# Performance work log

Measured on AMD Instinct MI355X. Metric: run time of the kernel, lower is better.

## Reference

```python
import jax, jax.numpy as jnp
import numpy as np
import math

B, T, E, H, QL, SUB = 4, 2048, 64, 8, 6, 64  # batch, win_len, n_embd, n_head, q_len, sub_len


def _row_mask(index, sub_len, win_len):
    log_l = math.ceil(np.log2(sub_len))
    mask = np.zeros(win_len, dtype=np.float32)
    if (win_len // sub_len) * 2 * log_l > index:
        mask[: index + 1] = 1
    else:
        while index >= 0:
            if index - log_l + 1 < 0:
                mask[:index] = 1
                break
            mask[index - log_l + 1 : index + 1] = 1
            for i in range(log_l):
                new_index = index - log_l + 1 - 2 ** i
                if index - new_index <= sub_len and new_index >= 0:
                    mask[new_index] = 1
            index -= sub_len
    return mask


def _log_mask(win_len, sub_len):
    m = np.zeros((win_len, win_len), dtype=np.float32)
    for i in range(win_len):
        m[i] = _row_mask(i, sub_len, win_len)
    return m.reshape(1, 1, win_len, win_len)


def setup_inputs() -> dict:
    key = jax.random.key(0)
    ks = jax.random.split(key, 4)
    x = jax.random.normal(ks[0], (B, T, E), dtype=jnp.float32)
    Wqk = jax.random.normal(ks[1], (2 * H * E, E, QL), dtype=jnp.float32) * 0.02
    bqk = jnp.zeros((2 * H * E,), dtype=jnp.float32)
    Wv = jax.random.normal(ks[2], (E, H * E), dtype=jnp.float32) * 0.02
    bv = jnp.zeros((H * E,), dtype=jnp.float32)
    Wp = jax.random.normal(ks[3], (H * E, E), dtype=jnp.float32) * 0.02
    bp = jnp.zeros((E,), dtype=jnp.float32)
    mask = jnp.asarray(_log_mask(T, SUB).astype(bool))  # [1,1,T,T] bool
    return {"x": x, "Wqk": Wqk, "bqk": bqk, "Wv": Wv, "bv": bv,
            "Wp": Wp, "bp": bp, "mask": mask}


def reference(x, Wqk, bqk, Wv, bv, Wp, bp, mask):
    b, t, e = x.shape
    h = Wv.shape[1] // e
    ql = Wqk.shape[-1]

    # value projection (Conv1D rf=1 == dense)
    value = x @ Wv + bv                              # [B,T,H*E]

    # causal conv1d QK projection: left-pad by q_len-1
    xc = jnp.transpose(x, (0, 2, 1))                 # [B,E,T]
    qk = jax.lax.conv_general_dilated(
        xc, Wqk, window_strides=(1,), padding=[(ql - 1, 0)],
        dimension_numbers=("NCH", "OIH", "NCH"))    # [B,2*H*E,T]
    qk = qk + bqk[None, :, None]
    qk = jnp.transpose(qk, (0, 2, 1))                # [B,T,2*H*E]
    query, key_ = jnp.split(qk, 2, axis=2)

    q = query.reshape(b, t, h, e).transpose(0, 2, 1, 3)   # [B,H,T,E]
    k = key_.reshape(b, t, h, e).transpose(0, 2, 3, 1)    # [B,H,E,T]
    v = value.reshape(b, t, h, e).transpose(0, 2, 1, 3)   # [B,H,T,E]

    pre = jnp.einsum("bhqe,bhek->bhqk", q, k) / jnp.sqrt(jnp.asarray(e, x.dtype))
    m = mask[:, :, :t, :t].astype(pre.dtype)
    pre = pre * m + (-1e9) * (1.0 - m)
    attn_weights = jax.nn.softmax(pre, axis=-1)           # [B,H,T,T]
    # dropout p=0.0 -> identity
    attn = jnp.einsum("bhqk,bhke->bhqe", attn_weights, v)  # [B,H,T,E]
    attn = attn.transpose(0, 2, 1, 3).reshape(b, t, h * e)
    out = attn @ Wp + bp                                  # [B,T,E]
    return out, attn_weights
```

## Files before the change

kernel.cpp:

```cpp
#include <hip/hip_runtime.h>
#include <hip/hip_bf16.h>


typedef __attribute__((ext_vector_type(8))) short bf16x8;
typedef __attribute__((ext_vector_type(4))) float f32x4;
typedef unsigned int uint32;

#define MFMA16(a, b, c) __builtin_amdgcn_mfma_f32_16x16x32_bf16((a), (b), (c), 0, 0, 0)

static __device__ __forceinline__ bool sparse_pred(int r, int c) {
  int d = r - c;
  if (d < 0) return false;
  int o = d & 63;
  int j = c + o;
  bool inS = (o <= 7) || (o == 9) || (o == 13) || (o == 21) || (o == 37);
  return (j >= 5) ? inS : (o >= 1);
}

static __device__ __forceinline__ uint32 bfbits(float x) {
  __hip_bfloat16 h = __float2bfloat16(x);
  unsigned short u;
  __builtin_memcpy(&u, &h, 2);
  return (uint32)u;
}

static __device__ __forceinline__ unsigned pred4(bool causal, int ct, int rt, int q, int nt,
                                                 int lq, const unsigned* pm4) {
  const int tb = ct * 64 + 16 * nt + 4 * lq;
  const int thr = q - tb;
  const unsigned cb = (thr < 0) ? 0u : (thr >= 3 ? 0xFu : (0xFu >> (3 - thr)));
  if (causal) return (ct < rt) ? 0xFu : cb;
  if (ct == 0) {
    unsigned p = 0;
#pragma unroll
    for (int reg = 0; reg < 4; ++reg) p |= (unsigned)sparse_pred(q, tb + reg) << reg;
    return p;
  }
  unsigned p = pm4[nt];
  if (ct == rt) p &= cb;
  return p;
}

struct KF {
  bf16x8 a[8];
};

static __device__ __forceinline__ KF loadK(const __hip_bfloat16* __restrict__ kbh, int ct, int lm,
                                           int lq) {
  KF f;
  const __hip_bfloat16* kbase = kbh + (size_t)ct * 64 * 64;
#pragma unroll
  for (int nb = 0; nb < 4; ++nb) {
    const __hip_bfloat16* krow = kbase + (size_t)(16 * nb + lm) * 64;
    f.a[2 * nb] = *reinterpret_cast<const bf16x8*>(krow + lq * 8);
    f.a[2 * nb + 1] = *reinterpret_cast<const bf16x8*>(krow + 32 + lq * 8);
  }
  return f;
}

struct VF {
  bf16x8 a[8];
};

static __device__ __forceinline__ VF loadV(const __hip_bfloat16* __restrict__ vbh, int ct, int lm,
                                           int lq) {
  VF f;
  const __hip_bfloat16* vbase = vbh + ct * 64;
#pragma unroll
  for (int eb = 0; eb < 4; ++eb) {
    const __hip_bfloat16* vrow = vbase + (size_t)(16 * eb + lm) * 2048;
    f.a[2 * eb] = *reinterpret_cast<const bf16x8*>(vrow + lq * 8);
    f.a[2 * eb + 1] = *reinterpret_cast<const bf16x8*>(vrow + 32 + lq * 8);
  }
  return f;
}

__global__ void prep_kernel(const float* __restrict__ Wqk, const float* __restrict__ Wv,
                            __hip_bfloat16* __restrict__ Wt_qk, __hip_bfloat16* __restrict__ Wv_t) {
  int idx = blockIdx.x * 256 + threadIdx.x;
  if (idx < 1024 * 384) {
    int o = idx / 384, kidx = idx - o * 384;
    int kk = kidx >> 6, i = kidx & 63;
    Wt_qk[idx] = __float2bfloat16(Wqk[(o * 64 + i) * 6 + kk]);
  } else {
    int j = idx - 1024 * 384;
    int n = j >> 6, k = j & 63;
    Wv_t[j] = __float2bfloat16(Wv[k * 512 + n]);
  }
}

__global__ __launch_bounds__(256, 4) void proj_kernel(
    const float* __restrict__ x, const float* __restrict__ bqk, const float* __restrict__ bv,
    const __hip_bfloat16* __restrict__ Wt_qk, const __hip_bfloat16* __restrict__ Wv_t,
    __hip_bfloat16* __restrict__ q_bf, __hip_bfloat16* __restrict__ k_bf,
    __hip_bfloat16* __restrict__ v_bf) {
  const int tokTile = blockIdx.x;
  const int chTile = blockIdx.y;
  const int gt0 = tokTile * 64;
  const int b = gt0 >> 11;
  const int t0 = gt0 & 2047;
  const int thr = threadIdx.x;
  __shared__ __align__(16) __hip_bfloat16 xwin[69][72];
  __shared__ __align__(16) __hip_bfloat16 vt[64][72];

  for (int u = thr; u < 69 * 64; u += 256) {
    int row = u >> 6, i = u & 63;
    int t = t0 - 5 + row;
    float v = (t >= 0) ? x[((size_t)b * 2048 + t) * 64 + i] : 0.f;
    xwin[row][i] = __float2bfloat16(v);
  }
  __syncthreads();

  const int wave = thr >> 6, lane = thr & 63;
  const int lm = lane & 15, lq = lane >> 4;
  f32x4 acc[4];
#pragma unroll
  for (int nb = 0; nb < 4; ++nb) acc[nb] = (f32x4){0.f, 0.f, 0.f, 0.f};

  if (chTile < 16) {
    const int ch0 = chTile * 64;
    for (int kc = 0; kc < 12; ++kc) {
      int k0 = kc * 32 + lq * 8;
      int kk = k0 >> 6, i0 = k0 & 63;
      bf16x8 a = *reinterpret_cast<const bf16x8*>(&xwin[16 * wave + lm + kk][i0]);
#pragma unroll
      for (int nb = 0; nb < 4; ++nb) {
        bf16x8 bb =
            *reinterpret_cast<const bf16x8*>(&Wt_qk[(size_t)(ch0 + 16 * nb + lm) * 384 + k0]);
        acc[nb] = MFMA16(a, bb, acc[nb]);
      }
    }
#pragma unroll
    for (int nb = 0; nb < 4; ++nb) {
      int e = 16 * nb + lm;
      float bias = bqk[chTile * 64 + e];
#pragma unroll
      for (int reg = 0; reg < 4; ++reg)
        vt[16 * wave + lq * 4 + reg][e] = __float2bfloat16(acc[nb][reg] + bias);
    }
    __syncthreads();
    const int half = (chTile >> 3) & 1;
    const int h = chTile & 7;
    __hip_bfloat16* dst = half ? k_bf : q_bf;
    for (int u = thr; u < 512; u += 256) {
      int row = u >> 3, c8 = u & 7;
      *reinterpret_cast<uint4*>(dst + ((size_t)((b * 8 + h) * 2048 + t0 + row)) * 64 + c8 * 8) =
          *reinterpret_cast<const uint4*>(&vt[row][c8 * 8]);
    }
  } else {
    const int nv0 = (chTile - 16) * 64;
    for (int kc = 0; kc < 2; ++kc) {
      int i0 = kc * 32 + lq * 8;
      bf16x8 a = *reinterpret_cast<const bf16x8*>(&xwin[16 * wave + lm + 5][i0]);
#pragma unroll
      for (int nb = 0; nb < 4; ++nb) {
        bf16x8 bb = *reinterpret_cast<const bf16x8*>(&Wv_t[(size_t)(nv0 + 16 * nb + lm) * 64 + i0]);
        acc[nb] = MFMA16(a, bb, acc[nb]);
      }
    }
#pragma unroll
    for (int nb = 0; nb < 4; ++nb) {
      int e = 16 * nb + lm;
      float bias = bv[nv0 + e];
#pragma unroll
      for (int reg = 0; reg < 4; ++reg)
        vt[e][16 * wave + lq * 4 + reg] = __float2bfloat16(acc[nb][reg] + bias);
    }
    __syncthreads();
    const int h = chTile - 16;
    for (int u = thr; u < 512; u += 256) {
      int e = u >> 3, c8 = u & 7;
      *reinterpret_cast<uint4*>(v_bf + ((size_t)((b * 8 + h) * 64 + e)) * 2048 + t0 + c8 * 8) =
          *reinterpret_cast<const uint4*>(&vt[e][c8 * 8]);
    }
  }
}

__global__ __launch_bounds__(256, 2) void attn_kernel(
    const __hip_bfloat16* __restrict__ q_bf, const __hip_bfloat16* __restrict__ k_bf,
    const __hip_bfloat16* __restrict__ v_bf,
    float* __restrict__ attn, float* __restrict__ attnout) {
  const int linear = (int)blockIdx.y * 16 + (int)blockIdx.x;
  const int xcd = linear & 7;
  const int slot = linear >> 3;
  const int bh = xcd * 4 + (slot >> 4);
  const int tb = slot & 15;
  const int wave = threadIdx.x >> 6;
  const int lane = threadIdx.x & 63;
  const int lm = lane & 15, lq = lane >> 4;

  __shared__ __align__(16) __hip_bfloat16 psw[4][16 * 72];
  __hip_bfloat16* pw = psw[wave];

  const int b2 = bh >> 3, h = bh & 7;
  const __hip_bfloat16* kbh = k_bf + (size_t)bh * 2048 * 64;
  const __hip_bfloat16* vbh = v_bf + (size_t)bh * 64 * 2048;

  const int q64 = 16 * wave + lm;
  unsigned pm4[4];
  {
    const int S[12] = {0, 1, 2, 3, 4, 5, 6, 7, 9, 13, 21, 37};
    unsigned long long M = 0;
#pragma unroll
    for (int i = 0; i < 12; ++i) M |= 1ull << ((q64 - S[i]) & 63);
#pragma unroll
    for (int nt = 0; nt < 4; ++nt) pm4[nt] = (unsigned)((M >> (16 * nt + 4 * lq)) & 0xFull);
  }

  for (int task = 0; task < 2; ++task) {
    const int rt = (task == 0) ? tb : 31 - tb;
    const int r0 = rt * 64;
    const bool causal = (rt < 6);
    const int q = r0 + q64;

    const __hip_bfloat16* qrow = q_bf + ((size_t)bh * 2048 + q) * 64;
    bf16x8 qa0 = *reinterpret_cast<const bf16x8*>(qrow + lq * 8);
    bf16x8 qa1 = *reinterpret_cast<const bf16x8*>(qrow + 32 + lq * 8);

    float lsum = 0.f;
    {
      KF kc = loadK(kbh, 0, lm, lq);
      for (int ct = 0; ct <= rt; ++ct) {
        KF kn = kc;
        if (ct < rt) kn = loadK(kbh, ct + 1, lm, lq);
#pragma unroll
        for (int nt = 0; nt < 4; ++nt) {
          f32x4 c = (f32x4){0.f, 0.f, 0.f, 0.f};
          c = MFMA16(kc.a[2 * nt], qa0, c);
          c = MFMA16(kc.a[2 * nt + 1], qa1, c);
          const unsigned p = pred4(causal, ct, rt, q, nt, lq, pm4);
#pragma unroll
          for (int reg = 0; reg < 4; ++reg)
            lsum += ((p >> reg) & 1u) ? __expf(c[reg] * 0.125f) : 0.f;
        }
        kc = kn;
      }
    }
    lsum += __shfl_xor(lsum, 16);
    lsum += __shfl_xor(lsum, 32);
    const float inv = 1.f / lsum;

    f32x4 oacc[4];
#pragma unroll
    for (int eb = 0; eb < 4; ++eb) oacc[eb] = (f32x4){0.f, 0.f, 0.f, 0.f};
    float* aq = attn + ((size_t)bh * 2048 + q) * 2048;

    KF kc = loadK(kbh, 0, lm, lq);
    VF vc = loadV(vbh, 0, lm, lq);
    for (int ct = 0; ct <= rt; ++ct) {
      KF kn = kc;
      VF vn = vc;
      if (ct < rt) {
        kn = loadK(kbh, ct + 1, lm, lq);
        vn = loadV(vbh, ct + 1, lm, lq);
      }
#pragma unroll
      for (int nt = 0; nt < 4; ++nt) {
        f32x4 c = (f32x4){0.f, 0.f, 0.f, 0.f};
        c = MFMA16(kc.a[2 * nt], qa0, c);
        c = MFMA16(kc.a[2 * nt + 1], qa1, c);
        const unsigned p = pred4(causal, ct, rt, q, nt, lq, pm4);
        f32x4 w;
#pragma unroll
        for (int reg = 0; reg < 4; ++reg)
          w[reg] = ((p >> reg) & 1u) ? __expf(c[reg] * 0.125f) * inv : 0.f;
        float* dst = aq + ct * 64 + 16 * nt + 4 * lq;
#pragma unroll
        for (int reg = 0; reg < 4; ++reg) __builtin_nontemporal_store(w[reg], dst + reg);
        uint32 u0 = bfbits(w[0]) | (bfbits(w[1]) << 16);
        uint32 u1 = bfbits(w[2]) | (bfbits(w[3]) << 16);
        uint2 uu = {u0, u1};
        *reinterpret_cast<uint2*>(&pw[lm * 72 + 16 * nt + 4 * lq]) = uu;
      }
      bf16x8 pa0 = *reinterpret_cast<const bf16x8*>(&pw[lm * 72 + lq * 8]);
      bf16x8 pa1 = *reinterpret_cast<const bf16x8*>(&pw[lm * 72 + 32 + lq * 8]);
#pragma unroll
      for (int eb = 0; eb < 4; ++eb) {
        oacc[eb] = MFMA16(vc.a[2 * eb], pa0, oacc[eb]);
        oacc[eb] = MFMA16(vc.a[2 * eb + 1], pa1, oacc[eb]);
      }
      kc = kn;
      vc = vn;
    }

    float* oq = attnout + ((size_t)(b2 * 2048 + q)) * 512 + h * 64;
#pragma unroll
    for (int eb = 0; eb < 4; ++eb)
      *reinterpret_cast<f32x4*>(oq + 16 * eb + 4 * lq) = oacc[eb];
  }
}

__global__ __launch_bounds__(256, 4) void outproj_kernel(const float* __restrict__ attnout,
                                                         const float* __restrict__ Wp,
                                                         const float* __restrict__ bp,
                                                         float* __restrict__ out) {
  __shared__ __align__(16) float wp_s[128][64];
  const int thr = threadIdx.x;
  const int wave = thr >> 6, lane = thr & 63;
  const int row0 = blockIdx.x * 16 + wave * 4;
  float acc[4] = {0.f, 0.f, 0.f, 0.f};
  for (int kt = 0; kt < 4; ++kt) {
    __syncthreads();
    for (int u = thr; u < 2048; u += 256) {
      int r = u >> 4, c4 = (u & 15) * 4;
      *reinterpret_cast<float4*>(&wp_s[r][c4]) =
          *reinterpret_cast<const float4*>(&Wp[(size_t)(kt * 128 + r) * 64 + c4]);
    }
    __syncthreads();
    for (int k4 = 0; k4 < 32; ++k4) {
      float wv0 = wp_s[k4 * 4 + 0][lane];
      float wv1 = wp_s[k4 * 4 + 1][lane];
      float wv2 = wp_s[k4 * 4 + 2][lane];
      float wv3 = wp_s[k4 * 4 + 3][lane];
#pragma unroll
      for (int rr = 0; rr < 4; ++rr) {
        const float4 a = *reinterpret_cast<const float4*>(
            &attnout[(size_t)(row0 + rr) * 512 + kt * 128 + k4 * 4]);
        acc[rr] += a.x * wv0 + a.y * wv1 + a.z * wv2 + a.w * wv3;
      }
    }
  }
  const float bias = bp[lane];
#pragma unroll
  for (int rr = 0; rr < 4; ++rr) out[(size_t)(row0 + rr) * 64 + lane] = acc[rr] + bias;
}

extern "C" void kernel_launch(void* const* d_in, const int* in_sizes, int n_in, void* d_out,
                              int out_size, void* d_ws, size_t ws_size, hipStream_t stream) {
  (void)in_sizes;
  (void)n_in;
  (void)out_size;
  (void)ws_size;
  const float* x = (const float*)d_in[0];
  const float* Wqk = (const float*)d_in[1];
  const float* bqk = (const float*)d_in[2];
  const float* Wv = (const float*)d_in[3];
  const float* bv = (const float*)d_in[4];
  const float* Wp = (const float*)d_in[5];
  const float* bp = (const float*)d_in[6];

  float* out = (float*)d_out;
  float* attn = out + (size_t)4 * 2048 * 64;

  char* ws = (char*)d_ws;
  __hip_bfloat16* q_bf = (__hip_bfloat16*)(ws);
  __hip_bfloat16* k_bf = (__hip_bfloat16*)(ws + (size_t)8 * 1024 * 1024);
  __hip_bfloat16* v_bf = (__hip_bfloat16*)(ws + (size_t)16 * 1024 * 1024);
  float* attnout = (float*)(ws + (size_t)24 * 1024 * 1024);
  __hip_bfloat16* Wt_qk = (__hip_bfloat16*)(ws + (size_t)40 * 1024 * 1024);
  __hip_bfloat16* Wv_t = (__hip_bfloat16*)(ws + (size_t)41 * 1024 * 1024);

  hipLaunchKernelGGL(prep_kernel, dim3(1664), dim3(256), 0, stream, Wqk, Wv, Wt_qk, Wv_t);
  hipLaunchKernelGGL(proj_kernel, dim3(128, 24), dim3(256), 0, stream, x, bqk, bv, Wt_qk, Wv_t,
                     q_bf, k_bf, v_bf);
  hipLaunchKernelGGL(attn_kernel, dim3(16, 32), dim3(256), 0, stream, q_bf, k_bf, v_bf, attn,
                     attnout);
  hipLaunchKernelGGL(outproj_kernel, dim3(512), dim3(256), 0, stream, attnout, Wp, bp, out);
}
```

Before: 745.4 us.

## Stage K/V tiles in double-buffered swizzled LDS shared across waves

Before, each wave loaded its own K and V fragments straight from global memory, so all four waves in a block read the same tile. Now the block cooperatively loads each 64x64 K and V tile once into a double-buffered, XOR-swizzled shared-memory buffer, prefetching the next tile into registers while computing the current one. Waves then read their fragments from LDS. The attention-weight stores are also merged into one 16-byte nontemporal vector store. The price is about 32KB more LDS per block, which may limit occupancy, plus a block barrier on every tile iteration.

```diff
diff --git a/kernel.cpp b/kernel.cpp
--- a/kernel.cpp
+++ b/kernel.cpp
@@ -39,40 +39,6 @@
   unsigned p = pm4[nt];
   if (ct == rt) p &= cb;
   return p;
-}
-
-struct KF {
-  bf16x8 a[8];
-};
-
-static __device__ __forceinline__ KF loadK(const __hip_bfloat16* __restrict__ kbh, int ct, int lm,
-                                           int lq) {
-  KF f;
-  const __hip_bfloat16* kbase = kbh + (size_t)ct * 64 * 64;
-#pragma unroll
-  for (int nb = 0; nb < 4; ++nb) {
-    const __hip_bfloat16* krow = kbase + (size_t)(16 * nb + lm) * 64;
-    f.a[2 * nb] = *reinterpret_cast<const bf16x8*>(krow + lq * 8);
-    f.a[2 * nb + 1] = *reinterpret_cast<const bf16x8*>(krow + 32 + lq * 8);
-  }
-  return f;
-}
-
-struct VF {
-  bf16x8 a[8];
-};
-
-static __device__ __forceinline__ VF loadV(const __hip_bfloat16* __restrict__ vbh, int ct, int lm,
-                                           int lq) {
-  VF f;
-  const __hip_bfloat16* vbase = vbh + ct * 64;
-#pragma unroll
-  for (int eb = 0; eb < 4; ++eb) {
-    const __hip_bfloat16* vrow = vbase + (size_t)(16 * eb + lm) * 2048;
-    f.a[2 * eb] = *reinterpret_cast<const bf16x8*>(vrow + lq * 8);
-    f.a[2 * eb + 1] = *reinterpret_cast<const bf16x8*>(vrow + 32 + lq * 8);
-  }
-  return f;
 }
 
 __global__ void prep_kernel(const float* __restrict__ Wqk, const float* __restrict__ Wv,
@@ -185,16 +151,33 @@
   const int slot = linear >> 3;
   const int bh = xcd * 4 + (slot >> 4);
   const int tb = slot & 15;
-  const int wave = threadIdx.x >> 6;
-  const int lane = threadIdx.x & 63;
+  const int tid = threadIdx.x;
+  const int wave = tid >> 6;
+  const int lane = tid & 63;
   const int lm = lane & 15, lq = lane >> 4;
 
+  __shared__ __align__(16) __hip_bfloat16 kbuf[2][4096];
+  __shared__ __align__(16) __hip_bfloat16 vbuf[2][4096];
   __shared__ __align__(16) __hip_bfloat16 psw[4][16 * 72];
   __hip_bfloat16* pw = psw[wave];
 
   const int b2 = bh >> 3, h = bh & 7;
-  const __hip_bfloat16* kbh = k_bf + (size_t)bh * 2048 * 64;
-  const __hip_bfloat16* vbh = v_bf + (size_t)bh * 64 * 2048;
+  const char* kbhB = (const char*)(k_bf + (size_t)bh * 2048 * 64);
+  const char* vbhB = (const char*)(v_bf + (size_t)bh * 64 * 2048);
+
+  int Ls[2], sK[2], sV[2];
+#pragma unroll
+  for (int i = 0; i < 2; ++i) {
+    const int L = i * 4096 + tid * 16;
+    const int r = L >> 7, c = L & 127;
+    const int cs = c ^ ((r & 7) << 4);
+    Ls[i] = L;
+    sK[i] = r * 128 + cs;
+    sV[i] = r * 4096 + cs;
+  }
+  const int fx = (lm & 7) << 4;
+  const int fc0 = (lq * 16) ^ fx;
+  const int fc1 = (64 + lq * 16) ^ fx;
 
   const int q64 = 16 * wave + lm;
   unsigned pm4[4];
@@ -217,24 +200,43 @@
     bf16x8 qa0 = *reinterpret_cast<const bf16x8*>(qrow + lq * 8);
     bf16x8 qa1 = *reinterpret_cast<const bf16x8*>(qrow + 32 + lq * 8);
 
+    uint4 ks0, ks1, vs0, vs1;
+
+    {
+      const char* kt = kbhB;
+      ks0 = *reinterpret_cast<const uint4*>(kt + sK[0]);
+      ks1 = *reinterpret_cast<const uint4*>(kt + sK[1]);
+      *reinterpret_cast<uint4*>((char*)kbuf[0] + Ls[0]) = ks0;
+      *reinterpret_cast<uint4*>((char*)kbuf[0] + Ls[1]) = ks1;
+    }
+    __syncthreads();
     float lsum = 0.f;
-    {
-      KF kc = loadK(kbh, 0, lm, lq);
-      for (int ct = 0; ct <= rt; ++ct) {
-        KF kn = kc;
-        if (ct < rt) kn = loadK(kbh, ct + 1, lm, lq);
-#pragma unroll
-        for (int nt = 0; nt < 4; ++nt) {
-          f32x4 c = (f32x4){0.f, 0.f, 0.f, 0.f};
-          c = MFMA16(kc.a[2 * nt], qa0, c);
-          c = MFMA16(kc.a[2 * nt + 1], qa1, c);
-          const unsigned p = pred4(causal, ct, rt, q, nt, lq, pm4);
-#pragma unroll
-          for (int reg = 0; reg < 4; ++reg)
-            lsum += ((p >> reg) & 1u) ? __expf(c[reg] * 0.125f) : 0.f;
-        }
-        kc = kn;
-      }
+    for (int ct = 0; ct <= rt; ++ct) {
+      if (ct < rt) {
+        const char* kt = kbhB + (size_t)(ct + 1) * 8192;
+        ks0 = *reinterpret_cast<const uint4*>(kt + sK[0]);
+        ks1 = *reinterpret_cast<const uint4*>(kt + sK[1]);
+      }
+      const char* kb = (const char*)kbuf[ct & 1];
+#pragma unroll
+      for (int nt = 0; nt < 4; ++nt) {
+        const int rb = (16 * nt + lm) * 128;
+        bf16x8 ka0 = *reinterpret_cast<const bf16x8*>(kb + rb + fc0);
+        bf16x8 ka1 = *reinterpret_cast<const bf16x8*>(kb + rb + fc1);
+        f32x4 c = (f32x4){0.f, 0.f, 0.f, 0.f};
+        c = MFMA16(ka0, qa0, c);
+        c = MFMA16(ka1, qa1, c);
+        const unsigned p = pred4(causal, ct, rt, q, nt, lq, pm4);
+#pragma unroll
+        for (int reg = 0; reg < 4; ++reg)
+          lsum += ((p >> reg) & 1u) ? __expf(c[reg] * 0.125f) : 0.f;
+      }
+      if (ct < rt) {
+        char* kw = (char*)kbuf[(ct + 1) & 1];
+        *reinterpret_cast<uint4*>(kw + Ls[0]) = ks0;
+        *reinterpret_cast<uint4*>(kw + Ls[1]) = ks1;
+      }
+      __syncthreads();
     }
     lsum += __shfl_xor(lsum, 16);
     lsum += __shfl_xor(lsum, 32);
@@ -245,28 +247,44 @@
     for (int eb = 0; eb < 4; ++eb) oacc[eb] = (f32x4){0.f, 0.f, 0.f, 0.f};
     float* aq = attn + ((size_t)bh * 2048 + q) * 2048;
 
-    KF kc = loadK(kbh, 0, lm, lq);
-    VF vc = loadV(vbh, 0, lm, lq);
+    {
+      const char* kt = kbhB;
+      ks0 = *reinterpret_cast<const uint4*>(kt + sK[0]);
+      ks1 = *reinterpret_cast<const uint4*>(kt + sK[1]);
+      const char* vt = vbhB;
+      vs0 = *reinterpret_cast<const uint4*>(vt + sV[0]);
+      vs1 = *reinterpret_cast<const uint4*>(vt + sV[1]);
+      *reinterpret_cast<uint4*>((char*)kbuf[0] + Ls[0]) = ks0;
+      *reinterpret_cast<uint4*>((char*)kbuf[0] + Ls[1]) = ks1;
+      *reinterpret_cast<uint4*>((char*)vbuf[0] + Ls[0]) = vs0;
+      *reinterpret_cast<uint4*>((char*)vbuf[0] + Ls[1]) = vs1;
+    }
+    __syncthreads();
     for (int ct = 0; ct <= rt; ++ct) {
-      KF kn = kc;
-      VF vn = vc;
       if (ct < rt) {
-        kn = loadK(kbh, ct + 1, lm, lq);
-        vn = loadV(vbh, ct + 1, lm, lq);
-      }
+        const char* kt = kbhB + (size_t)(ct + 1) * 8192;
+        ks0 = *reinterpret_cast<const uint4*>(kt + sK[0]);
+        ks1 = *reinterpret_cast<const uint4*>(kt + sK[1]);
+        const char* vt = vbhB + (size_t)(ct + 1) * 128;
+        vs0 = *reinterpret_cast<const uint4*>(vt + sV[0]);
+        vs1 = *reinterpret_cast<const uint4*>(vt + sV[1]);
+      }
+      const char* kb = (const char*)kbuf[ct & 1];
+      const char* vb = (const char*)vbuf[ct & 1];
 #pragma unroll
       for (int nt = 0; nt < 4; ++nt) {
+        const int rb = (16 * nt + lm) * 128;
+        bf16x8 ka0 = *reinterpret_cast<const bf16x8*>(kb + rb + fc0);
+        bf16x8 ka1 = *reinterpret_cast<const bf16x8*>(kb + rb + fc1);
         f32x4 c = (f32x4){0.f, 0.f, 0.f, 0.f};
-        c = MFMA16(kc.a[2 * nt], qa0, c);
-        c = MFMA16(kc.a[2 * nt + 1], qa1, c);
+        c = MFMA16(ka0, qa0, c);
+        c = MFMA16(ka1, qa1, c);
         const unsigned p = pred4(causal, ct, rt, q, nt, lq, pm4);
         f32x4 w;
 #pragma unroll
         for (int reg = 0; reg < 4; ++reg)
           w[reg] = ((p >> reg) & 1u) ? __expf(c[reg] * 0.125f) * inv : 0.f;
-        float* dst = aq + ct * 64 + 16 * nt + 4 * lq;
-#pragma unroll
-        for (int reg = 0; reg < 4; ++reg) __builtin_nontemporal_store(w[reg], dst + reg);
+        __builtin_nontemporal_store(w, reinterpret_cast<f32x4*>(aq + ct * 64 + 16 * nt + 4 * lq));
         uint32 u0 = bfbits(w[0]) | (bfbits(w[1]) << 16);
         uint32 u1 = bfbits(w[2]) | (bfbits(w[3]) << 16);
         uint2 uu = {u0, u1};
@@ -276,11 +294,21 @@
       bf16x8 pa1 = *reinterpret_cast<const bf16x8*>(&pw[lm * 72 + 32 + lq * 8]);
 #pragma unroll
       for (int eb = 0; eb < 4; ++eb) {
-        oacc[eb] = MFMA16(vc.a[2 * eb], pa0, oacc[eb]);
-        oacc[eb] = MFMA16(vc.a[2 * eb + 1], pa1, oacc[eb]);
-      }
-      kc = kn;
-      vc = vn;
+        const int rb = (16 * eb + lm) * 128;
+        bf16x8 va0 = *reinterpret_cast<const bf16x8*>(vb + rb + fc0);
+        bf16x8 va1 = *reinterpret_cast<const bf16x8*>(vb + rb + fc1);
+        oacc[eb] = MFMA16(va0, pa0, oacc[eb]);
+        oacc[eb] = MFMA16(va1, pa1, oacc[eb]);
+      }
+      if (ct < rt) {
+        char* kw = (char*)kbuf[(ct + 1) & 1];
+        *reinterpret_cast<uint4*>(kw + Ls[0]) = ks0;
+        *reinterpret_cast<uint4*>(kw + Ls[1]) = ks1;
+        char* vw = (char*)vbuf[(ct + 1) & 1];
+        *reinterpret_cast<uint4*>(vw + Ls[0]) = vs0;
+        *reinterpret_cast<uint4*>(vw + Ls[1]) = vs1;
+      }
+      __syncthreads();
     }
 
     float* oq = attnout + ((size_t)(b2 * 2048 + q)) * 512 + h * 64;
```

Measured after the change: 672.7 us (median of 2 runs). 9.7% less time.
